# Performance work log

Measured on AMD Instinct MI355X. Metric: run time of the kernel, lower is better.

The kernel has to match this reference:

```python
import jax, jax.numpy as jnp
import numpy as np

HOP = 5
NP_, NA_ = 100000, 100000


def spmm(src, dst, w, h, n_dst):
    # sparse.mm(A1, h): gather source rows, weight, scatter-add to destinations
    return jax.ops.segment_sum(h[src] * w[:, None], dst, num_segments=n_dst)


def sem_att(out, W1, b1, w2):
    # out: [N, R, D] stacked per-relation embeddings (HAN semantic attention)
    s = jnp.einsum('nrh,h->nr', jnp.tanh(jnp.einsum('nrd,dh->nrh', out, W1) + b1), w2)
    beta = jax.nn.softmax(jnp.mean(s, axis=0))  # [R]
    return jnp.einsum('nrd,r->nd', out, beta)


def setup_inputs() -> dict:
    key = jax.random.key(0)
    ks = jax.random.split(key, 32)
    E = 1600000
    inp = {
        'x_paper': jax.random.normal(ks[0], (NP_, 256), jnp.float32),
        'x_author': jax.random.normal(ks[1], (NA_, 128), jnp.float32),
        'fc1p_W': jax.random.normal(ks[2], (256, 128), jnp.float32) * 0.05,
        'fc1p_b': jnp.zeros((128,), jnp.float32),
        'fc1a_W': jax.random.normal(ks[3], (128, 128), jnp.float32) * 0.05,
        'fc1a_b': jnp.zeros((128,), jnp.float32),
        'fc2_W': jax.random.normal(ks[4], (128, 64), jnp.float32) * 0.05,
        'fc2_b': jnp.zeros((64,), jnp.float32),
        'semW1': jax.random.normal(ks[5], (HOP, 2, 128, 128), jnp.float32) * 0.05,
        'semb1': jnp.zeros((HOP, 2, 128), jnp.float32),
        'semw2': jax.random.normal(ks[6], (HOP, 2, 128), jnp.float32) * 0.05,
        'd_pp': jax.random.uniform(ks[7], (NP_, 1), jnp.float32),
        'd_pa': jax.random.uniform(ks[8], (NP_, 1), jnp.float32),
        'd_ap': jax.random.uniform(ks[9], (NA_, 1), jnp.float32),
        'd_aa': jax.random.uniform(ks[10], (NA_, 1), jnp.float32),
        'w_pp': jax.random.uniform(ks[11], (E,), jnp.float32) * 0.0625,
        'w_pa': jax.random.uniform(ks[12], (E,), jnp.float32) * 0.0625,
        'w_ap': jax.random.uniform(ks[13], (E,), jnp.float32) * 0.0625,
        'w_aa': jax.random.uniform(ks[14], (E,), jnp.float32) * 0.0625,
        'src_pp': jax.random.randint(ks[15], (E,), 0, NP_, jnp.int32),
        'dst_pp': jax.random.randint(ks[16], (E,), 0, NP_, jnp.int32),
        'src_pa': jax.random.randint(ks[17], (E,), 0, NA_, jnp.int32),
        'dst_pa': jax.random.randint(ks[18], (E,), 0, NP_, jnp.int32),
        'src_ap': jax.random.randint(ks[19], (E,), 0, NP_, jnp.int32),
        'dst_ap': jax.random.randint(ks[20], (E,), 0, NA_, jnp.int32),
        'src_aa': jax.random.randint(ks[21], (E,), 0, NA_, jnp.int32),
        'dst_aa': jax.random.randint(ks[22], (E,), 0, NA_, jnp.int32),
    }
    return inp


def reference(x_paper, x_author, fc1p_W, fc1p_b, fc1a_W, fc1a_b, fc2_W, fc2_b,
              semW1, semb1, semw2, d_pp, d_pa, d_ap, d_aa,
              w_pp, w_pa, w_ap, w_aa,
              src_pp, dst_pp, src_pa, dst_pa, src_ap, dst_ap, src_aa, dst_aa):
    # type-specific input projection (dropout is identity in eval mode)
    x_p = jax.nn.relu(x_paper @ fc1p_W + fc1p_b)   # [NP, H]
    x_a = jax.nn.relu(x_author @ fc1a_W + fc1a_b)  # [NA, H]
    h_p, h_a = x_p, x_a
    for i in range(HOP):
        # paper node type: relations (paper<-paper, paper<-author); uses old h_p, h_a
        hp_rel = jnp.stack([
            spmm(src_pp, dst_pp, w_pp, h_p, NP_) + d_pp * x_p,
            spmm(src_pa, dst_pa, w_pa, h_a, NP_) + d_pa * x_p,
        ], axis=1)  # [NP, 2, H]
        h_p = sem_att(hp_rel, semW1[i, 0], semb1[i, 0], semw2[i, 0])
        # author node type: relations (author<-paper, author<-author); uses updated h_p (sequential, as in torch)
        ha_rel = jnp.stack([
            spmm(src_ap, dst_ap, w_ap, h_p, NA_) + d_ap * x_a,
            spmm(src_aa, dst_aa, w_aa, h_a, NA_) + d_aa * x_a,
        ], axis=1)  # [NA, 2, H]
        h_a = sem_att(ha_rel, semW1[i, 1], semb1[i, 1], semw2[i, 1])
    return h_p @ fc2_W + fc2_b  # target_node_type = 'paper'
```

## Files before the change

kernel.cpp:

```cpp
#include <hip/hip_runtime.h>


typedef __attribute__((ext_vector_type(8))) short bf16x8;
typedef __attribute__((ext_vector_type(4))) float f32x4;
typedef __attribute__((ext_vector_type(4))) unsigned u32x4;
typedef __attribute__((ext_vector_type(2))) int i32x2;
typedef unsigned short ushort_t;

__device__ inline unsigned short f2bf(float f) {
  union { float f; unsigned u; } x; x.f = f;
  unsigned r = x.u + 0x7fff + ((x.u >> 16) & 1);
  return (unsigned short)(r >> 16);
}
__device__ inline float i2f(int i) {
  union { int i; float f; } x; x.i = i; return x.f;
}
__device__ inline int f2i(float f) {
  union { float f; int i; } x; x.f = f; return x.i;
}
__device__ inline void unpack8(u32x4 u, float* f) {
  union { unsigned u; float f; } c;
  c.u = u.x << 16;          f[0] = c.f;
  c.u = u.x & 0xffff0000u;  f[1] = c.f;
  c.u = u.y << 16;          f[2] = c.f;
  c.u = u.y & 0xffff0000u;  f[3] = c.f;
  c.u = u.z << 16;          f[4] = c.f;
  c.u = u.z & 0xffff0000u;  f[5] = c.f;
  c.u = u.w << 16;          f[6] = c.f;
  c.u = u.w & 0xffff0000u;  f[7] = c.f;
}
__device__ inline u32x4 pack8(const float* f) {
  u32x4 u;
  u.x = (unsigned)f2bf(f[0]) | ((unsigned)f2bf(f[1]) << 16);
  u.y = (unsigned)f2bf(f[2]) | ((unsigned)f2bf(f[3]) << 16);
  u.z = (unsigned)f2bf(f[4]) | ((unsigned)f2bf(f[5]) << 16);
  u.w = (unsigned)f2bf(f[6]) | ((unsigned)f2bf(f[7]) << 16);
  return u;
}

__global__ void zero_kernel(float* __restrict__ p, int n) {
  int i = blockIdx.x * blockDim.x + threadIdx.x;
  if (i < n) p[i] = 0.f;
}

struct Hist4Args {
  const int* dst[4];
  int* cnt[4];
  int E[4];
  int nb[4];
};

__global__ void hist4_kernel(Hist4Args a) {
  int vb = blockIdx.x;
#pragma unroll
  for (int r = 0; r < 4; r++) {
    if (vb < a.nb[r]) {
      int i = vb * 256 + threadIdx.x;
      if (i < a.E[r]) atomicAdd(&a.cnt[r][a.dst[r][i]], 1);
      return;
    }
    vb -= a.nb[r];
  }
}

__global__ void scan4_kernel(const int* __restrict__ cnt, int* __restrict__ rp,
                             int* __restrict__ cur, int Np, int Na) {
  __shared__ int wsum[16];
  __shared__ int carry_s;
  int r = blockIdx.x;
  int N = (r < 2) ? Np : Na;
  size_t coff  = (r==0)?0 : (r==1)? (size_t)Np : (r==2)? (size_t)2*Np : (size_t)2*Np+Na;
  size_t rpoff = (r==0)?0 : (r==1)? (size_t)(Np+1) : (r==2)? (size_t)2*(Np+1) : (size_t)2*(Np+1)+(Na+1);
  const int* c = cnt + coff;
  int* rpp = rp + rpoff;
  int* cpp = cur + coff;
  int tid = threadIdx.x;
  int lane = tid & 63, wv = tid >> 6;
  if (tid == 0) carry_s = 0;
  for (int base = 0; base < N; base += 1024) {
    int i = base + tid;
    int v = (i < N) ? c[i] : 0;
    int s = v;
#pragma unroll
    for (int off = 1; off < 64; off <<= 1) {
      int t = __shfl_up(s, off);
      if (lane >= off) s += t;
    }
    if (lane == 63) wsum[wv] = s;
    __syncthreads();
    if (wv == 0 && lane < 16) {
      int p = wsum[lane];
      int q = p;
#pragma unroll
      for (int off = 1; off < 16; off <<= 1) {
        int t = __shfl_up(q, off);
        if (lane >= off) q += t;
      }
      wsum[lane] = q - p;
    }
    __syncthreads();
    int carry = carry_s;
    int wexcl = wsum[wv];
    int excl = carry + wexcl + (s - v);
    if (i < N) { rpp[i] = excl; cpp[i] = excl; }
    int mytotal = wexcl + s;
    __syncthreads();
    if (tid == 1023) carry_s = carry + mytotal;
  }
  __syncthreads();
  if (tid == 0) rpp[N] = carry_s;
}

template<int K, int KH>
__device__ void fc1_body(float (*cstage)[16][128],
    const float* __restrict__ x, const float* __restrict__ W,
    const float* __restrict__ b, ushort_t* __restrict__ o1, ushort_t* __restrict__ o2,
    int N, int bid, int nblocks) {
  constexpr int TPB = 4 / KH;
  int tid = threadIdx.x;
  int lane = tid & 63, wid = tid >> 6;
  int tile = (KH == 2) ? (wid >> 1) : wid;
  int khalf = (KH == 2) ? (wid & 1) : 0;
  int r = lane & 15, kg = lane >> 4;
  bf16x8 bfr[8][4];
#pragma unroll
  for (int jt = 0; jt < 8; jt++) {
    int j = jt * 16 + r;
#pragma unroll
    for (int kt = 0; kt < 4; kt++) {
      int k0 = khalf * 128 + kt * 32 + kg * 8;
      bf16x8 v;
#pragma unroll
      for (int t = 0; t < 8; t++) v[t] = (short)f2bf(W[(size_t)(k0 + t) * 128 + j]);
      bfr[jt][kt] = v;
    }
  }
  float bb[8];
  {
    int j0 = (tid & 15) * 8;
#pragma unroll
    for (int t = 0; t < 8; t++) bb[t] = b[j0 + t];
  }
  int ntiles = (N + 15) >> 4;
  int tstride = nblocks * TPB;
  for (int tb = bid * TPB; tb < ntiles; tb += tstride) {
    int mytile = tb + tile;
    int nodeA = mytile * 16 + r;
    if (nodeA >= N) nodeA = 0;
    const float* xrow = x + (size_t)nodeA * K + khalf * 128;
    bf16x8 afr[4];
#pragma unroll
    for (int kt = 0; kt < 4; kt++) {
      const f32x4* p = (const f32x4*)(xrow + kt * 32 + kg * 8);
      f32x4 lo = __builtin_nontemporal_load(p);
      f32x4 hi = __builtin_nontemporal_load(p + 1);
      bf16x8 v;
      v[0] = (short)f2bf(lo.x); v[1] = (short)f2bf(lo.y);
      v[2] = (short)f2bf(lo.z); v[3] = (short)f2bf(lo.w);
      v[4] = (short)f2bf(hi.x); v[5] = (short)f2bf(hi.y);
      v[6] = (short)f2bf(hi.z); v[7] = (short)f2bf(hi.w);
      afr[kt] = v;
    }
    f32x4 acc[8];
#pragma unroll
    for (int jt = 0; jt < 8; jt++) acc[jt] = (f32x4){0.f, 0.f, 0.f, 0.f};
#pragma unroll
    for (int jt = 0; jt < 8; jt++)
#pragma unroll
      for (int kt = 0; kt < 4; kt++)
        acc[jt] = __builtin_amdgcn_mfma_f32_16x16x32_bf16(afr[kt], bfr[jt][kt], acc[jt], 0, 0, 0);
#pragma unroll
    for (int jt = 0; jt < 8; jt++)
#pragma unroll
      for (int reg = 0; reg < 4; reg++)
        cstage[wid][kg * 4 + reg][jt * 16 + r] = acc[jt][reg];
    __syncthreads();
    int node = tid >> 4, j0 = (tid & 15) * 8;
#pragma unroll
    for (int it = 0; it < TPB; it++) {
      int n = (tb + it) * 16 + node;
      float f[8];
#pragma unroll
      for (int t = 0; t < 8; t++) {
        float v = cstage[it * KH][node][j0 + t];
        if (KH == 2) v += cstage[it * 2 + 1][node][j0 + t];
        f[t] = fmaxf(v + bb[t], 0.f);
      }
      if (n < N) {
        u32x4 pk = pack8(f);
        *(u32x4*)(o1 + (size_t)n * 128 + j0) = pk;
        *(u32x4*)(o2 + (size_t)n * 128 + j0) = pk;
      }
    }
    __syncthreads();
  }
}

__device__ void scatter_body(const int* __restrict__ src, const int* __restrict__ dst,
                             const float* __restrict__ w, int* __restrict__ cur,
                             i32x2* __restrict__ cw, int E, int bid) {
  int i = bid * 256 + threadIdx.x;
  if (i < E) {
    int p = atomicAdd(&cur[dst[i]], 1);
    i32x2 v; v.x = src[i]; v.y = f2i(w[i]);
    cw[p] = v;
  }
}

struct BuildArgs {
  const float* fx[2]; const float* fW[2]; const float* fb[2];
  ushort_t* fo1[2]; ushort_t* fo2[2];
  int fN[2]; int fB[2];
  const int* src[4]; const int* dst[4]; const float* w[4];
  int* cur[4]; i32x2* cw[4];
  int E[4]; int nb[4];
};

__global__ __launch_bounds__(256) void build_kernel(BuildArgs a) {
  __shared__ float cstage[4][16][128];
  int vb = blockIdx.x;
  if (vb < a.fB[0]) {
    fc1_body<256, 2>(cstage, a.fx[0], a.fW[0], a.fb[0], a.fo1[0], a.fo2[0],
                     a.fN[0], vb, a.fB[0]);
    return;
  }
  vb -= a.fB[0];
  if (vb < a.fB[1]) {
    fc1_body<128, 1>(cstage, a.fx[1], a.fW[1], a.fb[1], a.fo1[1], a.fo2[1],
                     a.fN[1], vb, a.fB[1]);
    return;
  }
  vb -= a.fB[1];
#pragma unroll
  for (int r = 0; r < 4; r++) {
    if (vb < a.nb[r]) {
      scatter_body(a.src[r], a.dst[r], a.w[r], a.cur[r], a.cw[r], a.E[r], vb);
      return;
    }
    vb -= a.nb[r];
  }
}

__global__ __launch_bounds__(256) void spmm2_kernel(
    const ushort_t* __restrict__ xself,
    const float* __restrict__ d0, const float* __restrict__ d1,
    const ushort_t* __restrict__ h0, const ushort_t* __restrict__ h1,
    const int* __restrict__ rp0, const i32x2* __restrict__ cw0,
    const int* __restrict__ rp1, const i32x2* __restrict__ cw1,
    ushort_t* __restrict__ rel, int N) {
  int tid = threadIdx.x;
  int lane = tid & 63, wid = tid >> 6;
  int fg = lane & 15;
  int eslot = lane >> 4;
  int n = blockIdx.x * 4 + wid;
  if (n >= N) return;
  float xf[8];
  unpack8(*(const u32x4*)(xself + (size_t)n * 128 + fg * 8), xf);
#pragma unroll
  for (int srel = 0; srel < 2; srel++) {
    const float sd = srel ? d1[n] : d0[n];
    const int* rp = srel ? rp1 : rp0;
    const i32x2* cw = srel ? cw1 : cw0;
    const ushort_t* h = srel ? h1 : h0;
    float acc[8];
#pragma unroll
    for (int t = 0; t < 8; t++) acc[t] = 0.f;
    int beg = rp[n], end = rp[n + 1];
    for (int cb = beg; cb < end; cb += 64) {
      int m = end - cb; if (m > 64) m = 64;
      int creg = 0, wbits = 0;
      if (lane < m) {
        i32x2 p = __builtin_nontemporal_load(&cw[cb + lane]);
        creg = p.x; wbits = p.y;
      }
      int i = 0;
      for (; i + 16 <= m; i += 16) {
        int e0 = i + eslot, e1 = i + 4 + eslot, e2 = i + 8 + eslot, e3 = i + 12 + eslot;
        int   c0 = __shfl(creg, e0), c1 = __shfl(creg, e1);
        int   c2 = __shfl(creg, e2), c3 = __shfl(creg, e3);
        float v0 = i2f(__shfl(wbits, e0)), v1 = i2f(__shfl(wbits, e1));
        float v2 = i2f(__shfl(wbits, e2)), v3 = i2f(__shfl(wbits, e3));
        u32x4 g0 = *(const u32x4*)(h + (size_t)c0 * 128 + fg * 8);
        u32x4 g1 = *(const u32x4*)(h + (size_t)c1 * 128 + fg * 8);
        u32x4 g2 = *(const u32x4*)(h + (size_t)c2 * 128 + fg * 8);
        u32x4 g3 = *(const u32x4*)(h + (size_t)c3 * 128 + fg * 8);
        float hf[8];
        unpack8(g0, hf);
#pragma unroll
        for (int t = 0; t < 8; t++) acc[t] = fmaf(v0, hf[t], acc[t]);
        unpack8(g1, hf);
#pragma unroll
        for (int t = 0; t < 8; t++) acc[t] = fmaf(v1, hf[t], acc[t]);
        unpack8(g2, hf);
#pragma unroll
        for (int t = 0; t < 8; t++) acc[t] = fmaf(v2, hf[t], acc[t]);
        unpack8(g3, hf);
#pragma unroll
        for (int t = 0; t < 8; t++) acc[t] = fmaf(v3, hf[t], acc[t]);
      }
      for (; i < m; i += 4) {
        int e = i + eslot;
        int   c = __shfl(creg, e & 63);
        float v = i2f(__shfl(wbits, e & 63));
        if (e < m) {
          u32x4 g = *(const u32x4*)(h + (size_t)c * 128 + fg * 8);
          float hf[8];
          unpack8(g, hf);
#pragma unroll
          for (int t = 0; t < 8; t++) acc[t] = fmaf(v, hf[t], acc[t]);
        }
      }
    }
#pragma unroll
    for (int t = 0; t < 8; t++) {
      acc[t] += __shfl_xor(acc[t], 16);
      acc[t] += __shfl_xor(acc[t], 32);
    }
    if (eslot == 0) {
#pragma unroll
      for (int t = 0; t < 8; t++) acc[t] = fmaf(sd, xf[t], acc[t]);
      __builtin_nontemporal_store(pack8(acc),
          (u32x4*)(rel + (size_t)n * 256 + srel * 128 + fg * 8));
    }
  }
}

__global__ __launch_bounds__(256) void score_mfma_kernel(
    const ushort_t* __restrict__ rel,
    const float* __restrict__ W1,
    const float* __restrict__ b1, const float* __restrict__ w2,
    float* __restrict__ s_out, int N, int nwaves) {
  int tid = threadIdx.x;
  int lane = tid & 63;
  int gw = blockIdx.x * 4 + (tid >> 6);
  int r = lane & 15;
  int kg = lane >> 4;
  bf16x8 bfr[8][4];
#pragma unroll
  for (int jt = 0; jt < 8; jt++) {
    int j = jt * 16 + r;
#pragma unroll
    for (int kt = 0; kt < 4; kt++) {
      int k0 = kt * 32 + kg * 8;
      bf16x8 v;
#pragma unroll
      for (int t = 0; t < 8; t++) v[t] = (short)f2bf(W1[(size_t)(k0 + t) * 128 + j]);
      bfr[jt][kt] = v;
    }
  }
  float b1v[8], w2v[8];
#pragma unroll
  for (int jt = 0; jt < 8; jt++) { b1v[jt] = b1[jt * 16 + r]; w2v[jt] = w2[jt * 16 + r]; }
  float s0 = 0.f, s1 = 0.f;
  int ntiles = (N + 15) >> 4;
  for (int tile = gw; tile < ntiles; tile += nwaves) {
    int n0 = tile * 16;
    int nodeA = n0 + r;
    size_t base = (size_t)((nodeA < N) ? nodeA : 0) * 256;
#pragma unroll
    for (int sub = 0; sub < 2; sub++) {
      bf16x8 afr[4];
#pragma unroll
      for (int kt = 0; kt < 4; kt++)
        afr[kt] = __builtin_nontemporal_load(
            (const bf16x8*)(rel + base + sub * 128 + kt * 32 + kg * 8));
      f32x4 acc[8];
#pragma unroll
      for (int jt = 0; jt < 8; jt++) acc[jt] = (f32x4){0.f, 0.f, 0.f, 0.f};
#pragma unroll
      for (int jt = 0; jt < 8; jt++)
#pragma unroll
        for (int kt = 0; kt < 4; kt++)
          acc[jt] = __builtin_amdgcn_mfma_f32_16x16x32_bf16(afr[kt], bfr[jt][kt], acc[jt], 0, 0, 0);
      float sacc = 0.f;
#pragma unroll
      for (int jt = 0; jt < 8; jt++) {
#pragma unroll
        for (int reg = 0; reg < 4; reg++) {
          int nm = n0 + kg * 4 + reg;
          if (nm < N) sacc += w2v[jt] * tanhf(acc[jt][reg] + b1v[jt]);
        }
      }
      if (sub == 0) s0 += sacc; else s1 += sacc;
    }
  }
#pragma unroll
  for (int m = 32; m >= 1; m >>= 1) { s0 += __shfl_xor(s0, m); s1 += __shfl_xor(s1, m); }
  if (lane == 0) { atomicAdd(&s_out[0], s0); atomicAdd(&s_out[1], s1); }
}

__global__ void combine_kernel(const ushort_t* __restrict__ rel, const float* __restrict__ s,
                               ushort_t* __restrict__ h, int N, float invN) {
  int i = blockIdx.x * blockDim.x + threadIdx.x;
  if (i >= N * 16) return;
  float m0 = s[0] * invN, m1 = s[1] * invN;
  float mx = fmaxf(m0, m1);
  float e0 = expf(m0 - mx), e1 = expf(m1 - mx);
  float inv = 1.f / (e0 + e1);
  float be0 = e0 * inv, be1 = e1 * inv;
  int n = i >> 4, q = i & 15;
  float f0[8], f1[8], o[8];
  unpack8(__builtin_nontemporal_load((const u32x4*)(rel + (size_t)n * 256 + q * 8)), f0);
  unpack8(__builtin_nontemporal_load((const u32x4*)(rel + (size_t)n * 256 + 128 + q * 8)), f1);
#pragma unroll
  for (int t = 0; t < 8; t++) o[t] = be0 * f0[t] + be1 * f1[t];
  *(u32x4*)(h + (size_t)n * 128 + q * 8) = pack8(o);
}

__global__ __launch_bounds__(256) void fc2_mfma_kernel(
    const ushort_t* __restrict__ h,
    const float* __restrict__ W,
    const float* __restrict__ b,
    float* __restrict__ out, int N, int nwaves) {
  int tid = threadIdx.x;
  int lane = tid & 63;
  int gw = blockIdx.x * 4 + (tid >> 6);
  int r = lane & 15, kg = lane >> 4;
  bf16x8 bfr[4][4];
#pragma unroll
  for (int jt = 0; jt < 4; jt++) {
    int j = jt * 16 + r;
#pragma unroll
    for (int kt = 0; kt < 4; kt++) {
      int k0 = kt * 32 + kg * 8;
      bf16x8 v;
#pragma unroll
      for (int t = 0; t < 8; t++) v[t] = (short)f2bf(W[(size_t)(k0 + t) * 64 + j]);
      bfr[jt][kt] = v;
    }
  }
  float bv[4];
#pragma unroll
  for (int jt = 0; jt < 4; jt++) bv[jt] = b[jt * 16 + r];
  int ntiles = (N + 15) >> 4;
  for (int tile = gw; tile < ntiles; tile += nwaves) {
    int n0 = tile * 16;
    int nodeA = n0 + r;
    const ushort_t* hrow = h + (size_t)((nodeA < N) ? nodeA : 0) * 128;
    bf16x8 afr[4];
#pragma unroll
    for (int kt = 0; kt < 4; kt++)
      afr[kt] = *(const bf16x8*)(hrow + kt * 32 + kg * 8);
    f32x4 acc[4];
#pragma unroll
    for (int jt = 0; jt < 4; jt++) acc[jt] = (f32x4){0.f, 0.f, 0.f, 0.f};
#pragma unroll
    for (int jt = 0; jt < 4; jt++)
#pragma unroll
      for (int kt = 0; kt < 4; kt++)
        acc[jt] = __builtin_amdgcn_mfma_f32_16x16x32_bf16(afr[kt], bfr[jt][kt], acc[jt], 0, 0, 0);
#pragma unroll
    for (int jt = 0; jt < 4; jt++)
#pragma unroll
      for (int reg = 0; reg < 4; reg++) {
        int n = n0 + kg * 4 + reg;
        if (n < N) out[(size_t)n * 64 + jt * 16 + r] = acc[jt][reg] + bv[jt];
      }
  }
}

extern "C" void kernel_launch(void* const* d_in, const int* in_sizes, int n_in,
                              void* d_out, int out_size, void* d_ws, size_t ws_size,
                              hipStream_t stream) {
  const float* x_paper  = (const float*)d_in[0];
  const float* x_author = (const float*)d_in[1];
  const float* fc1p_W = (const float*)d_in[2];
  const float* fc1p_b = (const float*)d_in[3];
  const float* fc1a_W = (const float*)d_in[4];
  const float* fc1a_b = (const float*)d_in[5];
  const float* fc2_W  = (const float*)d_in[6];
  const float* fc2_b  = (const float*)d_in[7];
  const float* semW1  = (const float*)d_in[8];
  const float* semb1  = (const float*)d_in[9];
  const float* semw2  = (const float*)d_in[10];
  const float* d_pp = (const float*)d_in[11];
  const float* d_pa = (const float*)d_in[12];
  const float* d_ap = (const float*)d_in[13];
  const float* d_aa = (const float*)d_in[14];
  const float* w_pp = (const float*)d_in[15];
  const float* w_pa = (const float*)d_in[16];
  const float* w_ap = (const float*)d_in[17];
  const float* w_aa = (const float*)d_in[18];
  const int* src_pp = (const int*)d_in[19];
  const int* dst_pp = (const int*)d_in[20];
  const int* src_pa = (const int*)d_in[21];
  const int* dst_pa = (const int*)d_in[22];
  const int* src_ap = (const int*)d_in[23];
  const int* dst_ap = (const int*)d_in[24];
  const int* src_aa = (const int*)d_in[25];
  const int* dst_aa = (const int*)d_in[26];

  const int Np = in_sizes[11];
  const int Na = in_sizes[13];
  const int E[4] = { in_sizes[15], in_sizes[16], in_sizes[17], in_sizes[18] };
  const int Nmax = (Np > Na) ? Np : Na;

  char* base = (char*)d_ws;
  size_t off = 0;
  ushort_t* xp = (ushort_t*)(base + off); off += (size_t)Np * 128 * 2;
  ushort_t* xa = (ushort_t*)(base + off); off += (size_t)Na * 128 * 2;
  ushort_t* hp = (ushort_t*)(base + off); off += (size_t)Np * 128 * 2;
  ushort_t* ha = (ushort_t*)(base + off); off += (size_t)Na * 128 * 2;
  ushort_t* rel = (ushort_t*)(base + off); off += (size_t)Nmax * 256 * 2;
  float* ssum = (float*)(base + off); off += 32 * 4;
  int* cnt  = (int*)(base + off); off += (size_t)(2 * Np + 2 * Na) * 4;
  int* rpB  = (int*)(base + off); off += (size_t)(2 * (Np + 1) + 2 * (Na + 1)) * 4;
  int* curB = (int*)(base + off); off += (size_t)(2 * Np + 2 * Na) * 4;
  size_t Esum = (size_t)E[0] + E[1] + E[2] + E[3];
  off = (off + 15) & ~(size_t)15;
  i32x2* cwB = (i32x2*)(base + off); off += Esum * 8;
  (void)ws_size; (void)n_in; (void)out_size;

  int* cnt_r[4] = { cnt, cnt + Np, cnt + (size_t)2 * Np, cnt + (size_t)2 * Np + Na };
  int* rp_r[4]  = { rpB, rpB + (Np + 1), rpB + (size_t)2 * (Np + 1),
                    rpB + (size_t)2 * (Np + 1) + (Na + 1) };
  int* cur_r[4] = { curB, curB + Np, curB + (size_t)2 * Np, curB + (size_t)2 * Np + Na };
  size_t eoff[4] = { 0, (size_t)E[0], (size_t)E[0] + E[1], (size_t)E[0] + E[1] + E[2] };
  i32x2* cw_r[4];
  for (int r = 0; r < 4; r++) cw_r[r] = cwB + eoff[r];

  const int* srcs[4]    = { src_pp, src_pa, src_ap, src_aa };
  const int* dsts[4]    = { dst_pp, dst_pa, dst_ap, dst_aa };
  const float* wedge[4] = { w_pp, w_pa, w_ap, w_aa };

  int Z = 32 + 2 * Np + 2 * Na;
  zero_kernel<<<(Z + 255) / 256, 256, 0, stream>>>(ssum, Z);

  Hist4Args ha_args;
  int hist_blocks = 0;
  for (int r = 0; r < 4; r++) {
    ha_args.dst[r] = dsts[r];
    ha_args.cnt[r] = cnt_r[r];
    ha_args.E[r] = E[r];
    ha_args.nb[r] = (E[r] + 255) / 256;
    hist_blocks += ha_args.nb[r];
  }
  hist4_kernel<<<hist_blocks, 256, 0, stream>>>(ha_args);

  scan4_kernel<<<4, 1024, 0, stream>>>(cnt, rpB, curB, Np, Na);

  BuildArgs ba;
  ba.fx[0] = x_paper;  ba.fW[0] = fc1p_W; ba.fb[0] = fc1p_b;
  ba.fo1[0] = xp; ba.fo2[0] = hp; ba.fN[0] = Np; ba.fB[0] = 256;
  ba.fx[1] = x_author; ba.fW[1] = fc1a_W; ba.fb[1] = fc1a_b;
  ba.fo1[1] = xa; ba.fo2[1] = ha; ba.fN[1] = Na; ba.fB[1] = 256;
  int build_blocks = ba.fB[0] + ba.fB[1];
  for (int r = 0; r < 4; r++) {
    ba.src[r] = srcs[r]; ba.dst[r] = dsts[r]; ba.w[r] = wedge[r];
    ba.cur[r] = cur_r[r]; ba.cw[r] = cw_r[r]; ba.E[r] = E[r];
    ba.nb[r] = (E[r] + 255) / 256;
    build_blocks += ba.nb[r];
  }
  build_kernel<<<build_blocks, 256, 0, stream>>>(ba);

  const int SCORE_BLOCKS = 256;
  const int SCORE_WAVES = SCORE_BLOCKS * 4;

  for (int i = 0; i < 5; i++) {
    float* sp = ssum + (size_t)(i * 2 + 0) * 2;
    spmm2_kernel<<<(Np + 3) / 4, 256, 0, stream>>>(xp, d_pp, d_pa, hp, ha,
        rp_r[0], cw_r[0], rp_r[1], cw_r[1], rel, Np);
    score_mfma_kernel<<<SCORE_BLOCKS, 256, 0, stream>>>(rel,
        semW1 + (size_t)(i * 2 + 0) * 16384, semb1 + (size_t)(i * 2 + 0) * 128,
        semw2 + (size_t)(i * 2 + 0) * 128, sp, Np, SCORE_WAVES);
    combine_kernel<<<(Np * 16 + 255) / 256, 256, 0, stream>>>(rel, sp, hp, Np, 1.f / Np);

    if (i < 4) {
      float* sa = ssum + (size_t)(i * 2 + 1) * 2;
      spmm2_kernel<<<(Na + 3) / 4, 256, 0, stream>>>(xa, d_ap, d_aa, hp, ha,
          rp_r[2], cw_r[2], rp_r[3], cw_r[3], rel, Na);
      score_mfma_kernel<<<SCORE_BLOCKS, 256, 0, stream>>>(rel,
          semW1 + (size_t)(i * 2 + 1) * 16384, semb1 + (size_t)(i * 2 + 1) * 128,
          semw2 + (size_t)(i * 2 + 1) * 128, sa, Na, SCORE_WAVES);
      combine_kernel<<<(Na * 16 + 255) / 256, 256, 0, stream>>>(rel, sa, ha, Na, 1.f / Na);
    }
  }

  fc2_mfma_kernel<<<256, 256, 0, stream>>>(hp, fc2_W, fc2_b, (float*)d_out, Np, 1024);
}
```

Before: 2.508 ms.

## Fuse semantic-attention scoring into SpMM kernel and rebalance fc1 across prep kernels

The score computation is fused into the SpMM kernel. Each block now handles 16 nodes, stages their bf16 relation rows in LDS and runs the W1 MFMA plus tanh and w2 reduction on that tile, so rel is no longer re-read from global memory. Block partial sums go to 16 atomic slots, which combine_kernel then sums. The paper fc1 projection moves into the histogram kernel so it overlaps with the atomic counting, leaving only the author fc1 in build_kernel. The cost is that every block re-converts its W1 slice from fp32 to bf16, and the SpMM kernel uses more LDS and registers, which may reduce occupancy.

```diff
diff --git a/kernel.cpp b/kernel.cpp
--- a/kernel.cpp
+++ b/kernel.cpp
@@ -41,26 +41,6 @@
 __global__ void zero_kernel(float* __restrict__ p, int n) {
   int i = blockIdx.x * blockDim.x + threadIdx.x;
   if (i < n) p[i] = 0.f;
-}
-
-struct Hist4Args {
-  const int* dst[4];
-  int* cnt[4];
-  int E[4];
-  int nb[4];
-};
-
-__global__ void hist4_kernel(Hist4Args a) {
-  int vb = blockIdx.x;
-#pragma unroll
-  for (int r = 0; r < 4; r++) {
-    if (vb < a.nb[r]) {
-      int i = vb * 256 + threadIdx.x;
-      if (i < a.E[r]) atomicAdd(&a.cnt[r][a.dst[r][i]], 1);
-      return;
-    }
-    vb -= a.nb[r];
-  }
 }
 
 __global__ void scan4_kernel(const int* __restrict__ cnt, int* __restrict__ rp,
@@ -196,6 +176,31 @@
   }
 }
 
+struct PrepArgs {
+  const float* fx; const float* fW; const float* fb;
+  ushort_t* fo1; ushort_t* fo2; int fN; int fB;
+  const int* dst[4]; int* cnt[4]; int E[4]; int nb[4];
+};
+
+__global__ __launch_bounds__(256) void prep_kernel(PrepArgs a) {
+  __shared__ float cstage[4][16][128];
+  int vb = blockIdx.x;
+  if (vb < a.fB) {
+    fc1_body<256, 2>(cstage, a.fx, a.fW, a.fb, a.fo1, a.fo2, a.fN, vb, a.fB);
+    return;
+  }
+  vb -= a.fB;
+#pragma unroll
+  for (int r = 0; r < 4; r++) {
+    if (vb < a.nb[r]) {
+      int i = vb * 256 + threadIdx.x;
+      if (i < a.E[r]) atomicAdd(&a.cnt[r][a.dst[r][i]], 1);
+      return;
+    }
+    vb -= a.nb[r];
+  }
+}
+
 __device__ void scatter_body(const int* __restrict__ src, const int* __restrict__ dst,
                              const float* __restrict__ w, int* __restrict__ cur,
                              i32x2* __restrict__ cw, int E, int bid) {
@@ -208,9 +213,8 @@
 }
 
 struct BuildArgs {
-  const float* fx[2]; const float* fW[2]; const float* fb[2];
-  ushort_t* fo1[2]; ushort_t* fo2[2];
-  int fN[2]; int fB[2];
+  const float* fx; const float* fW; const float* fb;
+  ushort_t* fo1; ushort_t* fo2; int fN; int fB;
   const int* src[4]; const int* dst[4]; const float* w[4];
   int* cur[4]; i32x2* cw[4];
   int E[4]; int nb[4];
@@ -219,18 +223,11 @@
 __global__ __launch_bounds__(256) void build_kernel(BuildArgs a) {
   __shared__ float cstage[4][16][128];
   int vb = blockIdx.x;
-  if (vb < a.fB[0]) {
-    fc1_body<256, 2>(cstage, a.fx[0], a.fW[0], a.fb[0], a.fo1[0], a.fo2[0],
-                     a.fN[0], vb, a.fB[0]);
+  if (vb < a.fB) {
+    fc1_body<128, 1>(cstage, a.fx, a.fW, a.fb, a.fo1, a.fo2, a.fN, vb, a.fB);
     return;
   }
-  vb -= a.fB[0];
-  if (vb < a.fB[1]) {
-    fc1_body<128, 1>(cstage, a.fx[1], a.fW[1], a.fb[1], a.fo1[1], a.fo2[1],
-                     a.fN[1], vb, a.fB[1]);
-    return;
-  }
-  vb -= a.fB[1];
+  vb -= a.fB;
 #pragma unroll
   for (int r = 0; r < 4; r++) {
     if (vb < a.nb[r]) {
@@ -241,159 +238,172 @@
   }
 }
 
-__global__ __launch_bounds__(256) void spmm2_kernel(
+__global__ __launch_bounds__(256) void spmm2s_kernel(
     const ushort_t* __restrict__ xself,
     const float* __restrict__ d0, const float* __restrict__ d1,
     const ushort_t* __restrict__ h0, const ushort_t* __restrict__ h1,
     const int* __restrict__ rp0, const i32x2* __restrict__ cw0,
     const int* __restrict__ rp1, const i32x2* __restrict__ cw1,
-    ushort_t* __restrict__ rel, int N) {
+    ushort_t* __restrict__ rel, int N,
+    const float* __restrict__ W1, const float* __restrict__ b1,
+    const float* __restrict__ w2, float* __restrict__ s_slots) {
+  __shared__ ushort_t lrel[16][2][132];
+  __shared__ float red[4][2];
   int tid = threadIdx.x;
   int lane = tid & 63, wid = tid >> 6;
   int fg = lane & 15;
   int eslot = lane >> 4;
-  int n = blockIdx.x * 4 + wid;
-  if (n >= N) return;
-  float xf[8];
-  unpack8(*(const u32x4*)(xself + (size_t)n * 128 + fg * 8), xf);
-#pragma unroll
-  for (int srel = 0; srel < 2; srel++) {
-    const float sd = srel ? d1[n] : d0[n];
-    const int* rp = srel ? rp1 : rp0;
-    const i32x2* cw = srel ? cw1 : cw0;
-    const ushort_t* h = srel ? h1 : h0;
-    float acc[8];
-#pragma unroll
-    for (int t = 0; t < 8; t++) acc[t] = 0.f;
-    int beg = rp[n], end = rp[n + 1];
-    for (int cb = beg; cb < end; cb += 64) {
-      int m = end - cb; if (m > 64) m = 64;
-      int creg = 0, wbits = 0;
-      if (lane < m) {
-        i32x2 p = __builtin_nontemporal_load(&cw[cb + lane]);
-        creg = p.x; wbits = p.y;
-      }
-      int i = 0;
-      for (; i + 16 <= m; i += 16) {
-        int e0 = i + eslot, e1 = i + 4 + eslot, e2 = i + 8 + eslot, e3 = i + 12 + eslot;
-        int   c0 = __shfl(creg, e0), c1 = __shfl(creg, e1);
-        int   c2 = __shfl(creg, e2), c3 = __shfl(creg, e3);
-        float v0 = i2f(__shfl(wbits, e0)), v1 = i2f(__shfl(wbits, e1));
-        float v2 = i2f(__shfl(wbits, e2)), v3 = i2f(__shfl(wbits, e3));
-        u32x4 g0 = *(const u32x4*)(h + (size_t)c0 * 128 + fg * 8);
-        u32x4 g1 = *(const u32x4*)(h + (size_t)c1 * 128 + fg * 8);
-        u32x4 g2 = *(const u32x4*)(h + (size_t)c2 * 128 + fg * 8);
-        u32x4 g3 = *(const u32x4*)(h + (size_t)c3 * 128 + fg * 8);
-        float hf[8];
-        unpack8(g0, hf);
-#pragma unroll
-        for (int t = 0; t < 8; t++) acc[t] = fmaf(v0, hf[t], acc[t]);
-        unpack8(g1, hf);
-#pragma unroll
-        for (int t = 0; t < 8; t++) acc[t] = fmaf(v1, hf[t], acc[t]);
-        unpack8(g2, hf);
-#pragma unroll
-        for (int t = 0; t < 8; t++) acc[t] = fmaf(v2, hf[t], acc[t]);
-        unpack8(g3, hf);
-#pragma unroll
-        for (int t = 0; t < 8; t++) acc[t] = fmaf(v3, hf[t], acc[t]);
-      }
-      for (; i < m; i += 4) {
-        int e = i + eslot;
-        int   c = __shfl(creg, e & 63);
-        float v = i2f(__shfl(wbits, e & 63));
-        if (e < m) {
-          u32x4 g = *(const u32x4*)(h + (size_t)c * 128 + fg * 8);
+  int n0 = blockIdx.x * 16;
+  for (int s = 0; s < 4; s++) {
+    int node_slot = wid * 4 + s;
+    int n = n0 + node_slot;
+    bool valid = n < N;
+    float xf[8];
+    if (valid) unpack8(*(const u32x4*)(xself + (size_t)n * 128 + fg * 8), xf);
+#pragma unroll
+    for (int srel = 0; srel < 2; srel++) {
+      float sd = 0.f;
+      int beg = 0, end = 0;
+      const i32x2* cw = srel ? cw1 : cw0;
+      const ushort_t* h = srel ? h1 : h0;
+      if (valid) {
+        sd = srel ? d1[n] : d0[n];
+        const int* rp = srel ? rp1 : rp0;
+        beg = rp[n]; end = rp[n + 1];
+      }
+      float acc[8];
+#pragma unroll
+      for (int t = 0; t < 8; t++) acc[t] = 0.f;
+      for (int cb = beg; cb < end; cb += 64) {
+        int m = end - cb; if (m > 64) m = 64;
+        int creg = 0, wbits = 0;
+        if (lane < m) {
+          i32x2 p = __builtin_nontemporal_load(&cw[cb + lane]);
+          creg = p.x; wbits = p.y;
+        }
+        int i = 0;
+        for (; i + 16 <= m; i += 16) {
+          int e0 = i + eslot, e1 = i + 4 + eslot, e2 = i + 8 + eslot, e3 = i + 12 + eslot;
+          int   c0 = __shfl(creg, e0), c1 = __shfl(creg, e1);
+          int   c2 = __shfl(creg, e2), c3 = __shfl(creg, e3);
+          float v0 = i2f(__shfl(wbits, e0)), v1 = i2f(__shfl(wbits, e1));
+          float v2 = i2f(__shfl(wbits, e2)), v3 = i2f(__shfl(wbits, e3));
+          u32x4 g0 = *(const u32x4*)(h + (size_t)c0 * 128 + fg * 8);
+          u32x4 g1 = *(const u32x4*)(h + (size_t)c1 * 128 + fg * 8);
+          u32x4 g2 = *(const u32x4*)(h + (size_t)c2 * 128 + fg * 8);
+          u32x4 g3 = *(const u32x4*)(h + (size_t)c3 * 128 + fg * 8);
           float hf[8];
-          unpack8(g, hf);
-#pragma unroll
-          for (int t = 0; t < 8; t++) acc[t] = fmaf(v, hf[t], acc[t]);
+          unpack8(g0, hf);
+#pragma unroll
+          for (int t = 0; t < 8; t++) acc[t] = fmaf(v0, hf[t], acc[t]);
+          unpack8(g1, hf);
+#pragma unroll
+          for (int t = 0; t < 8; t++) acc[t] = fmaf(v1, hf[t], acc[t]);
+          unpack8(g2, hf);
+#pragma unroll
+          for (int t = 0; t < 8; t++) acc[t] = fmaf(v2, hf[t], acc[t]);
+          unpack8(g3, hf);
+#pragma unroll
+          for (int t = 0; t < 8; t++) acc[t] = fmaf(v3, hf[t], acc[t]);
         }
-      }
-    }
-#pragma unroll
-    for (int t = 0; t < 8; t++) {
-      acc[t] += __shfl_xor(acc[t], 16);
-      acc[t] += __shfl_xor(acc[t], 32);
-    }
-    if (eslot == 0) {
-#pragma unroll
-      for (int t = 0; t < 8; t++) acc[t] = fmaf(sd, xf[t], acc[t]);
-      __builtin_nontemporal_store(pack8(acc),
-          (u32x4*)(rel + (size_t)n * 256 + srel * 128 + fg * 8));
-    }
-  }
-}
-
-__global__ __launch_bounds__(256) void score_mfma_kernel(
-    const ushort_t* __restrict__ rel,
-    const float* __restrict__ W1,
-    const float* __restrict__ b1, const float* __restrict__ w2,
-    float* __restrict__ s_out, int N, int nwaves) {
-  int tid = threadIdx.x;
-  int lane = tid & 63;
-  int gw = blockIdx.x * 4 + (tid >> 6);
-  int r = lane & 15;
-  int kg = lane >> 4;
-  bf16x8 bfr[8][4];
-#pragma unroll
-  for (int jt = 0; jt < 8; jt++) {
-    int j = jt * 16 + r;
+        for (; i < m; i += 4) {
+          int e = i + eslot;
+          int   c = __shfl(creg, e & 63);
+          float v = i2f(__shfl(wbits, e & 63));
+          if (e < m) {
+            u32x4 g = *(const u32x4*)(h + (size_t)c * 128 + fg * 8);
+            float hf[8];
+            unpack8(g, hf);
+#pragma unroll
+            for (int t = 0; t < 8; t++) acc[t] = fmaf(v, hf[t], acc[t]);
+          }
+        }
+      }
+#pragma unroll
+      for (int t = 0; t < 8; t++) {
+        acc[t] += __shfl_xor(acc[t], 16);
+        acc[t] += __shfl_xor(acc[t], 32);
+      }
+      if (eslot == 0) {
+        if (valid) {
+#pragma unroll
+          for (int t = 0; t < 8; t++) acc[t] = fmaf(sd, xf[t], acc[t]);
+        } else {
+#pragma unroll
+          for (int t = 0; t < 8; t++) acc[t] = 0.f;
+        }
+        u32x4 pk = pack8(acc);
+        *(u32x4*)(&lrel[node_slot][srel][fg * 8]) = pk;
+        if (valid)
+          __builtin_nontemporal_store(pk,
+              (u32x4*)(rel + (size_t)n * 256 + srel * 128 + fg * 8));
+      }
+    }
+  }
+  __syncthreads();
+  int r = lane & 15, kg = lane >> 4;
+  bf16x8 bfr[2][4];
+  float b1v[2], w2v[2];
+#pragma unroll
+  for (int q = 0; q < 2; q++) {
+    int j = (wid * 2 + q) * 16 + r;
+    b1v[q] = b1[j]; w2v[q] = w2[j];
 #pragma unroll
     for (int kt = 0; kt < 4; kt++) {
       int k0 = kt * 32 + kg * 8;
       bf16x8 v;
 #pragma unroll
       for (int t = 0; t < 8; t++) v[t] = (short)f2bf(W1[(size_t)(k0 + t) * 128 + j]);
-      bfr[jt][kt] = v;
-    }
-  }
-  float b1v[8], w2v[8];
-#pragma unroll
-  for (int jt = 0; jt < 8; jt++) { b1v[jt] = b1[jt * 16 + r]; w2v[jt] = w2[jt * 16 + r]; }
+      bfr[q][kt] = v;
+    }
+  }
   float s0 = 0.f, s1 = 0.f;
-  int ntiles = (N + 15) >> 4;
-  for (int tile = gw; tile < ntiles; tile += nwaves) {
-    int n0 = tile * 16;
-    int nodeA = n0 + r;
-    size_t base = (size_t)((nodeA < N) ? nodeA : 0) * 256;
-#pragma unroll
-    for (int sub = 0; sub < 2; sub++) {
-      bf16x8 afr[4];
+#pragma unroll
+  for (int sub = 0; sub < 2; sub++) {
+    bf16x8 afr[4];
+#pragma unroll
+    for (int kt = 0; kt < 4; kt++)
+      afr[kt] = *(const bf16x8*)(&lrel[r][sub][kt * 32 + kg * 8]);
+    f32x4 acc2[2];
+#pragma unroll
+    for (int q = 0; q < 2; q++) acc2[q] = (f32x4){0.f, 0.f, 0.f, 0.f};
+#pragma unroll
+    for (int q = 0; q < 2; q++)
 #pragma unroll
       for (int kt = 0; kt < 4; kt++)
-        afr[kt] = __builtin_nontemporal_load(
-            (const bf16x8*)(rel + base + sub * 128 + kt * 32 + kg * 8));
-      f32x4 acc[8];
-#pragma unroll
-      for (int jt = 0; jt < 8; jt++) acc[jt] = (f32x4){0.f, 0.f, 0.f, 0.f};
-#pragma unroll
-      for (int jt = 0; jt < 8; jt++)
-#pragma unroll
-        for (int kt = 0; kt < 4; kt++)
-          acc[jt] = __builtin_amdgcn_mfma_f32_16x16x32_bf16(afr[kt], bfr[jt][kt], acc[jt], 0, 0, 0);
-      float sacc = 0.f;
-#pragma unroll
-      for (int jt = 0; jt < 8; jt++) {
-#pragma unroll
-        for (int reg = 0; reg < 4; reg++) {
-          int nm = n0 + kg * 4 + reg;
-          if (nm < N) sacc += w2v[jt] * tanhf(acc[jt][reg] + b1v[jt]);
-        }
-      }
-      if (sub == 0) s0 += sacc; else s1 += sacc;
-    }
+        acc2[q] = __builtin_amdgcn_mfma_f32_16x16x32_bf16(afr[kt], bfr[q][kt], acc2[q], 0, 0, 0);
+    float sacc = 0.f;
+#pragma unroll
+    for (int q = 0; q < 2; q++) {
+#pragma unroll
+      for (int reg = 0; reg < 4; reg++) {
+        int nm = n0 + kg * 4 + reg;
+        if (nm < N) sacc += w2v[q] * tanhf(acc2[q][reg] + b1v[q]);
+      }
+    }
+    if (sub == 0) s0 = sacc; else s1 = sacc;
   }
 #pragma unroll
   for (int m = 32; m >= 1; m >>= 1) { s0 += __shfl_xor(s0, m); s1 += __shfl_xor(s1, m); }
-  if (lane == 0) { atomicAdd(&s_out[0], s0); atomicAdd(&s_out[1], s1); }
+  if (lane == 0) { red[wid][0] = s0; red[wid][1] = s1; }
+  __syncthreads();
+  if (tid == 0) {
+    float t0 = red[0][0] + red[1][0] + red[2][0] + red[3][0];
+    float t1 = red[0][1] + red[1][1] + red[2][1] + red[3][1];
+    int slot = blockIdx.x & 15;
+    atomicAdd(&s_slots[slot], t0);
+    atomicAdd(&s_slots[16 + slot], t1);
+  }
 }
 
 __global__ void combine_kernel(const ushort_t* __restrict__ rel, const float* __restrict__ s,
                                ushort_t* __restrict__ h, int N, float invN) {
   int i = blockIdx.x * blockDim.x + threadIdx.x;
   if (i >= N * 16) return;
-  float m0 = s[0] * invN, m1 = s[1] * invN;
+  float t0 = 0.f, t1 = 0.f;
+#pragma unroll
+  for (int k = 0; k < 16; k++) { t0 += s[k]; t1 += s[16 + k]; }
+  float m0 = t0 * invN, m1 = t1 * invN;
   float mx = fmaxf(m0, m1);
   float e0 = expf(m0 - mx), e1 = expf(m1 - mx);
   float inv = 1.f / (e0 + e1);
@@ -502,7 +512,7 @@
   ushort_t* hp = (ushort_t*)(base + off); off += (size_t)Np * 128 * 2;
   ushort_t* ha = (ushort_t*)(base + off); off += (size_t)Na * 128 * 2;
   ushort_t* rel = (ushort_t*)(base + off); off += (size_t)Nmax * 256 * 2;
-  float* ssum = (float*)(base + off); off += 32 * 4;
+  float* ssum = (float*)(base + off); off += 1024 * 4;
   int* cnt  = (int*)(base + off); off += (size_t)(2 * Np + 2 * Na) * 4;
   int* rpB  = (int*)(base + off); off += (size_t)(2 * (Np + 1) + 2 * (Na + 1)) * 4;
   int* curB = (int*)(base + off); off += (size_t)(2 * Np + 2 * Na) * 4;
@@ -523,28 +533,28 @@
   const int* dsts[4]    = { dst_pp, dst_pa, dst_ap, dst_aa };
   const float* wedge[4] = { w_pp, w_pa, w_ap, w_aa };
 
-  int Z = 32 + 2 * Np + 2 * Na;
+  int Z = 1024 + 2 * Np + 2 * Na;
   zero_kernel<<<(Z + 255) / 256, 256, 0, stream>>>(ssum, Z);
 
-  Hist4Args ha_args;
-  int hist_blocks = 0;
+  PrepArgs pa_args;
+  pa_args.fx = x_paper; pa_args.fW = fc1p_W; pa_args.fb = fc1p_b;
+  pa_args.fo1 = xp; pa_args.fo2 = hp; pa_args.fN = Np; pa_args.fB = 256;
+  int prep_blocks = 256;
   for (int r = 0; r < 4; r++) {
-    ha_args.dst[r] = dsts[r];
-    ha_args.cnt[r] = cnt_r[r];
-    ha_args.E[r] = E[r];
-    ha_args.nb[r] = (E[r] + 255) / 256;
-    hist_blocks += ha_args.nb[r];
-  }
-  hist4_kernel<<<hist_blocks, 256, 0, stream>>>(ha_args);
+    pa_args.dst[r] = dsts[r];
+    pa_args.cnt[r] = cnt_r[r];
+    pa_args.E[r] = E[r];
+    pa_args.nb[r] = (E[r] + 255) / 256;
+    prep_blocks += pa_args.nb[r];
+  }
+  prep_kernel<<<prep_blocks, 256, 0, stream>>>(pa_args);
 
   scan4_kernel<<<4, 1024, 0, stream>>>(cnt, rpB, curB, Np, Na);
 
   BuildArgs ba;
-  ba.fx[0] = x_paper;  ba.fW[0] = fc1p_W; ba.fb[0] = fc1p_b;
-  ba.fo1[0] = xp; ba.fo2[0] = hp; ba.fN[0] = Np; ba.fB[0] = 256;
-  ba.fx[1] = x_author; ba.fW[1] = fc1a_W; ba.fb[1] = fc1a_b;
-  ba.fo1[1] = xa; ba.fo2[1] = ha; ba.fN[1] = Na; ba.fB[1] = 256;
-  int build_blocks = ba.fB[0] + ba.fB[1];
+  ba.fx = x_author; ba.fW = fc1a_W; ba.fb = fc1a_b;
+  ba.fo1 = xa; ba.fo2 = ha; ba.fN = Na; ba.fB = 256;
+  int build_blocks = 256;
   for (int r = 0; r < 4; r++) {
     ba.src[r] = srcs[r]; ba.dst[r] = dsts[r]; ba.w[r] = wedge[r];
     ba.cur[r] = cur_r[r]; ba.cw[r] = cw_r[r]; ba.E[r] = E[r];
@@ -553,25 +563,20 @@
   }
   build_kernel<<<build_blocks, 256, 0, stream>>>(ba);
 
-  const int SCORE_BLOCKS = 256;
-  const int SCORE_WAVES = SCORE_BLOCKS * 4;
-
   for (int i = 0; i < 5; i++) {
-    float* sp = ssum + (size_t)(i * 2 + 0) * 2;
-    spmm2_kernel<<<(Np + 3) / 4, 256, 0, stream>>>(xp, d_pp, d_pa, hp, ha,
-        rp_r[0], cw_r[0], rp_r[1], cw_r[1], rel, Np);
-    score_mfma_kernel<<<SCORE_BLOCKS, 256, 0, stream>>>(rel,
+    float* sp = ssum + (size_t)(i * 2 + 0) * 32;
+    spmm2s_kernel<<<(Np + 15) / 16, 256, 0, stream>>>(xp, d_pp, d_pa, hp, ha,
+        rp_r[0], cw_r[0], rp_r[1], cw_r[1], rel, Np,
         semW1 + (size_t)(i * 2 + 0) * 16384, semb1 + (size_t)(i * 2 + 0) * 128,
-        semw2 + (size_t)(i * 2 + 0) * 128, sp, Np, SCORE_WAVES);
+        semw2 + (size_t)(i * 2 + 0) * 128, sp);
     combine_kernel<<<(Np * 16 + 255) / 256, 256, 0, stream>>>(rel, sp, hp, Np, 1.f / Np);
 
     if (i < 4) {
-      float* sa = ssum + (size_t)(i * 2 + 1) * 2;
-      spmm2_kernel<<<(Na + 3) / 4, 256, 0, stream>>>(xa, d_ap, d_aa, hp, ha,
-          rp_r[2], cw_r[2], rp_r[3], cw_r[3], rel, Na);
-      score_mfma_kernel<<<SCORE_BLOCKS, 256, 0, stream>>>(rel,
+      float* sa = ssum + (size_t)(i * 2 + 1) * 32;
+      spmm2s_kernel<<<(Na + 15) / 16, 256, 0, stream>>>(xa, d_ap, d_aa, hp, ha,
+          rp_r[2], cw_r[2], rp_r[3], cw_r[3], rel, Na,
           semW1 + (size_t)(i * 2 + 1) * 16384, semb1 + (size_t)(i * 2 + 1) * 128,
-          semw2 + (size_t)(i * 2 + 1) * 128, sa, Na, SCORE_WAVES);
+          semw2 + (size_t)(i * 2 + 1) * 128, sa);
       combine_kernel<<<(Na * 16 + 255) / 256, 256, 0, stream>>>(rel, sa, ha, Na, 1.f / Na);
     }
   }
```

Measured after the change: 2.713 ms. 1.08x slower.
